# Performance work log

Hardware: AMD Instinct MI355X
Metric: run time of the kernel (lower is better)

Reference implementation:

```python
import jax, jax.numpy as jnp
import numpy as np

EPS = 1e-5
ROPE_BASE = 10000.0
N_HEAD = 16


def rms_norm(x, eps=EPS):
    return x * jax.lax.rsqrt(jnp.mean(x * x, axis=-1, keepdims=True) + eps)


def rope(x):
    # x: [B, H, L, D]; non-standard interleaved variant from the source:
    # x_odd = x[..., 1::2], x_even = x[..., ::2]
    # y = interleave(y_odd, y_even)
    B, H, L, D = x.shape
    inv_freq = 1.0 / (ROPE_BASE ** (jnp.arange(0, D, 2, dtype=jnp.float32) / D))
    angles = jnp.arange(L, dtype=jnp.float32)[:, None] * inv_freq[None, :]  # [L, D/2]
    cos, sin = jnp.cos(angles), jnp.sin(angles)
    x_odd = x[..., 1::2].astype(jnp.float32)
    x_even = x[..., ::2].astype(jnp.float32)
    y_odd = x_odd * cos - x_even * sin
    y_even = x_odd * sin + x_even * cos
    y = jnp.stack([y_odd, y_even], axis=-1).reshape(B, H, L, D)
    return y.astype(x.dtype)


def setup_inputs() -> dict:
    key = jax.random.key(0)
    k1, k2, k3 = jax.random.split(key, 3)
    B, L, HID = 2, 2048, 2048
    in_std = 0.5 * HID ** (-0.5)
    bound = (3 ** 0.5) * in_std
    x = jax.random.normal(k1, (B, L, HID), dtype=jnp.float32)
    W_qkv = jax.random.uniform(k2, (3 * HID, HID), minval=-bound, maxval=bound, dtype=jnp.float32)
    # out_proj is zero-initialized in the source; use small random weights so the
    # output (and gradients) are non-trivial for correctness checking.
    W_out = jax.random.uniform(k3, (HID, HID), minval=-bound, maxval=bound, dtype=jnp.float32)
    return {"x": x, "W_qkv": W_qkv, "W_out": W_out}


def reference(x, W_qkv, W_out):
    B, L, HID = x.shape
    D = HID // N_HEAD
    qkv = jnp.einsum('blc,fc->blf', x, W_qkv)  # [B, L, 3*HID]
    q, k, v = jnp.split(qkv, 3, axis=-1)
    def heads(t):
        return t.reshape(B, L, N_HEAD, D).transpose(0, 2, 1, 3)  # [B,H,L,D]
    q, k, v = heads(q), heads(k), heads(v)
    q = rope(rms_norm(q))
    k = rope(rms_norm(k))
    scale = 1.0 / jnp.sqrt(jnp.asarray(D, dtype=jnp.float32))
    scores = jnp.einsum('bhqd,bhkd->bhqk', q, k) * scale
    causal = jnp.tril(jnp.ones((L, L), dtype=bool))
    scores = jnp.where(causal, scores, -jnp.inf)
    attn = jax.nn.softmax(scores, axis=-1)
    out = jnp.einsum('bhqk,bhkd->bhqd', attn, v)
    out = out.transpose(0, 2, 1, 3).reshape(B, L, HID)
    return jnp.einsum('blc,fc->blf', out, W_out)
```

## Files before the change

kernel.cpp:

```cpp
#include <hip/hip_runtime.h>
#include <stdint.h>
#include <math.h>

typedef unsigned short u16;
typedef unsigned int u32;
typedef __attribute__((ext_vector_type(8))) short bf16x8;
typedef __attribute__((ext_vector_type(4))) float f32x4;

#define SEQ 2048
#define HID 2048
#define NH  16
#define DH  128
#define NB  2

typedef __attribute__((address_space(1))) const u32 gu32;
typedef __attribute__((address_space(3))) u32 lu32;

__device__ __forceinline__ u16 f2bf(float f) {
  u32 u = __float_as_uint(f);
  return (u16)((u + 0x7fffu + ((u >> 16) & 1u)) >> 16);
}
__device__ __forceinline__ float bf2f(u16 h) { return __uint_as_float(((u32)h) << 16); }

__device__ __forceinline__ void gload_lds16(const void* g, void* l) {
  __builtin_amdgcn_global_load_lds((gu32*)g, (lu32*)l, 16, 0, 0);
}

__global__ __launch_bounds__(256) void k_cvt3(const float* __restrict__ s0, u16* __restrict__ d0, int n0,
                                              const float* __restrict__ s1, u16* __restrict__ d1, int n1,
                                              const float* __restrict__ s2, u16* __restrict__ d2, int n2) {
  int i = blockIdx.x * 256 + threadIdx.x;
  int stride = gridDim.x * 256;
  int total = n0 + n1 + n2;
  for (; i < total; i += stride) {
    const float* s; u16* d; int k = i;
    if (k < n0) { s = s0; d = d0; }
    else if (k < n0 + n1) { s = s1; d = d1; k -= n0; }
    else { s = s2; d = d2; k -= n0 + n1; }
    float4 v = ((const float4*)s)[k];
    ushort4 o;
    o.x = f2bf(v.x); o.y = f2bf(v.y); o.z = f2bf(v.z); o.w = f2bf(v.w);
    ((ushort4*)d)[k] = o;
  }
}

template<int EPI>
__global__ __launch_bounds__(256)
void k_gemm(const u16* __restrict__ A, const u16* __restrict__ Bm,
            float* __restrict__ Cf, u16* __restrict__ Qr, u16* __restrict__ Kr, u16* __restrict__ Vr,
            int N, int K, int NX) {
  __shared__ alignas(16) char sA[128 * 128];
  __shared__ alignas(16) char sB[128 * 128];
  const int tid = threadIdx.x;
  const int wid = tid >> 6, lane = tid & 63;
  const int l15 = lane & 15, l4 = lane >> 4;
  const int nwg = gridDim.x, bid = blockIdx.x;
  const int wg = (bid & 7) * (nwg >> 3) + (bid >> 3);
  const int bx = wg % NX, by = wg / NX;
  const int m0 = by * 128, n0 = bx * 128;
  const int wr = (wid >> 1) * 64, wc = (wid & 1) * 64;

  f32x4 acc[4][4];
  #pragma unroll
  for (int i = 0; i < 4; ++i)
    #pragma unroll
    for (int j = 0; j < 4; ++j)
      acc[i][j] = (f32x4){0.f, 0.f, 0.f, 0.f};

  const int nkt = K >> 6;
  for (int kt = 0; kt < nkt; ++kt) {
    const int k0 = kt << 6;
    __syncthreads();
    #pragma unroll
    for (int it = 0; it < 4; ++it) {
      int o = it * 4096 + tid * 16;
      int row = o >> 7, cb = o & 127;
      int scb = cb ^ ((row & 7) << 4);
      gload_lds16((const char*)A + ((size_t)(m0 + row) * K + k0) * 2 + scb, &sA[it * 4096 + wid * 1024]);
    }
    #pragma unroll
    for (int it = 0; it < 4; ++it) {
      int o = it * 4096 + tid * 16;
      int row = o >> 7, cb = o & 127;
      int scb = cb ^ ((row & 7) << 4);
      gload_lds16((const char*)Bm + ((size_t)(n0 + row) * K + k0) * 2 + scb, &sB[it * 4096 + wid * 1024]);
    }
    __syncthreads();
    #pragma unroll
    for (int kk = 0; kk < 2; ++kk) {
      bf16x8 av[4], bv[4];
      #pragma unroll
      for (int mi = 0; mi < 4; ++mi) {
        int row = wr + mi * 16 + l15;
        int colb = kk * 64 + 16 * l4;
        av[mi] = *(const bf16x8*)&sA[row * 128 + (colb ^ ((row & 7) << 4))];
      }
      #pragma unroll
      for (int ni = 0; ni < 4; ++ni) {
        int row = wc + ni * 16 + l15;
        int colb = kk * 64 + 16 * l4;
        bv[ni] = *(const bf16x8*)&sB[row * 128 + (colb ^ ((row & 7) << 4))];
      }
      #pragma unroll
      for (int mi = 0; mi < 4; ++mi)
        #pragma unroll
        for (int ni = 0; ni < 4; ++ni)
          acc[mi][ni] = __builtin_amdgcn_mfma_f32_16x16x32_bf16(av[mi], bv[ni], acc[mi][ni], 0, 0, 0);
    }
  }

  #pragma unroll
  for (int mi = 0; mi < 4; ++mi) {
    #pragma unroll
    for (int ni = 0; ni < 4; ++ni) {
      #pragma unroll
      for (int j = 0; j < 4; ++j) {
        int gm = m0 + wr + mi * 16 + l4 * 4 + j;
        int gn = n0 + wc + ni * 16 + l15;
        float v = acc[mi][ni][j];
        if (EPI == 0) {
          int b = gm >> 11, l = gm & 2047;
          int which = gn >> 11, hid = gn & 2047;
          int h = hid >> 7, d = hid & 127;
          u16* dst = (which == 0) ? Qr : ((which == 1) ? Kr : Vr);
          size_t idx = ((size_t)(b * NH + h) * SEQ + l) * DH + d;
          dst[idx] = f2bf(v);
        } else {
          Cf[(size_t)gm * N + gn] = v;
        }
      }
    }
  }
}

__global__ __launch_bounds__(256) void k_vtr(const u16* __restrict__ Vr, u16* __restrict__ Vt) {
  __shared__ u16 tile[64][72];
  const int k0 = blockIdx.x * 64, d0 = blockIdx.y * 64, bh = blockIdx.z;
  const u16* src = Vr + ((size_t)bh << 18);
  u16* dst = Vt + ((size_t)bh << 18);
  const int tid = threadIdx.x;
  #pragma unroll
  for (int it = 0; it < 2; ++it) {
    int e = it * 2048 + tid * 8;
    int r = e >> 6, c = e & 63;
    bf16x8 v = *(const bf16x8*)(src + (size_t)(k0 + r) * DH + d0 + c);
    *(bf16x8*)&tile[r][c] = v;
  }
  __syncthreads();
  #pragma unroll
  for (int it = 0; it < 2; ++it) {
    int e = it * 2048 + tid * 8;
    int rd = e >> 6, ck = e & 63;
    bf16x8 w;
    #pragma unroll
    for (int i = 0; i < 8; ++i) w[i] = (short)tile[ck + i][rd];
    *(bf16x8*)(dst + (size_t)(d0 + rd) * SEQ + k0 + ck) = w;
  }
}

__global__ __launch_bounds__(256) void k_nrope2(u16* __restrict__ Qr, u16* __restrict__ Kr, float mq) {
  u16* T = blockIdx.y ? Kr : Qr;
  const float mul = blockIdx.y ? 1.0f : mq;
  const int r = blockIdx.x * 4 + (threadIdx.x >> 6);
  const int lane = threadIdx.x & 63;
  u16* p = T + ((size_t)r << 7) + lane * 2;
  u32 pr = *(const u32*)p;
  float xe = bf2f((u16)(pr & 0xffffu));
  float xo = bf2f((u16)(pr >> 16));
  float ss = xe * xe + xo * xo;
  #pragma unroll
  for (int off = 1; off < 64; off <<= 1) ss += __shfl_xor(ss, off);
  float rinv = rsqrtf(ss * (1.f / 128.f) + 1e-5f);
  float e = xe * rinv, o = xo * rinv;
  int pos = r & (SEQ - 1);
  float freq = exp2f(-0.20762050593046014f * (float)lane);
  float ang = (float)pos * freq;
  float sn, cs;
  sincosf(ang, &sn, &cs);
  u32 outw = (u32)f2bf((o * cs - e * sn) * mul) | ((u32)f2bf((o * sn + e * cs) * mul) << 16);
  *(u32*)p = outw;
}


__device__ __forceinline__ void smax(f32x4 (&sacc)[4], float& m_, float& se,
                                     f32x4* accO, u32 (&pw)[8],
                                     bool diag, int qpos, int kb, int l15, int l4) {
  if (diag) {
    #pragma unroll
    for (int sj = 0; sj < 4; ++sj)
      #pragma unroll
      for (int j = 0; j < 4; ++j) {
        int kpos = kb + sj * 16 + l4 * 4 + j;
        if (kpos > qpos) sacc[sj][j] = -1e30f;
      }
  }
  float mx = sacc[0][0];
  #pragma unroll
  for (int sj = 0; sj < 4; ++sj)
    #pragma unroll
    for (int j = 0; j < 4; ++j) mx = fmaxf(mx, sacc[sj][j]);
  mx = fmaxf(mx, __shfl_xor(mx, 16));
  mx = fmaxf(mx, __shfl_xor(mx, 32));
  if (!__all(mx <= m_ + 8.f)) {
    float mn = fmaxf(m_, mx);
    float corr = __builtin_exp2f(m_ - mn);
    m_ = mn;
    se *= corr;
    float corr4[4];
    #pragma unroll
    for (int j = 0; j < 4; ++j) corr4[j] = __shfl(corr, l4 * 4 + j);
    #pragma unroll
    for (int db = 0; db < 8; ++db) {
      f32x4 a = accO[db];
      #pragma unroll
      for (int j = 0; j < 4; ++j) a[j] *= corr4[j];
      accO[db] = a;
    }
  }
  float sum = 0.f;
  #pragma unroll
  for (int sj = 0; sj < 4; ++sj)
    #pragma unroll
    for (int jp = 0; jp < 2; ++jp) {
      float p0 = __builtin_exp2f(sacc[sj][jp * 2]     - m_);
      float p1 = __builtin_exp2f(sacc[sj][jp * 2 + 1] - m_);
      pw[sj * 2 + jp] = (u32)f2bf(p0) | ((u32)f2bf(p1) << 16);
      sum += p0 + p1;
    }
  sum += __shfl_xor(sum, 16);
  sum += __shfl_xor(sum, 32);
  se += sum;
}

__device__ __forceinline__ void pwrite(char* sPw, const u32 (&pw)[8], int l15, int l4) {
  const int sw = (l15 & 7) << 4;
  char* base = sPw + l15 * 128;
  #pragma unroll
  for (int sj = 0; sj < 4; ++sj)
    #pragma unroll
    for (int jp = 0; jp < 2; ++jp)
      *(u32*)(base + ((sj * 32 + l4 * 8 + jp * 4) ^ sw)) = pw[sj * 2 + jp];
}

__device__ __forceinline__ void stage_kv(const char* Kp, const char* Vtp, int kb,
                                         char* bK, char* bV, int tid, int wid) {
  #pragma unroll
  for (int it = 0; it < 4; ++it) {
    int o = it * 4096 + tid * 16;
    int row = o >> 8, cb = o & 255;
    int scb = cb ^ ((row & 7) << 4);
    gload_lds16(Kp + (size_t)(kb + row) * 256 + scb, &bK[it * 4096 + wid * 1024]);
  }
  #pragma unroll
  for (int it = 0; it < 4; ++it) {
    int o = it * 4096 + tid * 16;
    int row = o >> 7, cb = o & 127;
    int scb = cb ^ ((row & 7) << 4);
    gload_lds16(Vtp + (size_t)row * (SEQ * 2) + kb * 2 + scb, &bV[it * 4096 + wid * 1024]);
  }
}

__global__ __launch_bounds__(256, 2)
void k_attn(const u16* __restrict__ Q, const u16* __restrict__ Kg,
            const u16* __restrict__ Vt, u16* __restrict__ O) {
  __shared__ alignas(16) char sK0[64 * 256];
  __shared__ alignas(16) char sK1[64 * 256];
  __shared__ alignas(16) char sV0[128 * 128];
  __shared__ alignas(16) char sV1[128 * 128];
  __shared__ alignas(16) char sP[4 * 2048];
  const int tid = threadIdx.x, wid = tid >> 6, lane = tid & 63;
  const int l15 = lane & 15, l4 = lane >> 4;
  const int i = blockIdx.x;
  const int xcd = i & 7, slot = i >> 3;
  const int p = slot & 15;
  const int bh = xcd + 8 * (slot >> 4);
  const int b = bh >> 4, h = bh & 15;
  const int tA = p, tB = 31 - p;
  const u16* Qp = Q + ((size_t)bh << 18);
  const char* Kp = (const char*)(Kg + ((size_t)bh << 18));
  const char* Vtp = (const char*)(Vt + ((size_t)bh << 18));
  const int q0A = tA * 64 + wid * 16;
  const int q0B = tB * 64 + wid * 16;

  bf16x8 aqA[4], aqB[4];
  #pragma unroll
  for (int kk = 0; kk < 4; ++kk) {
    aqA[kk] = *(const bf16x8*)(Qp + (size_t)(q0A + l15) * DH + kk * 32 + 8 * l4);
    aqB[kk] = *(const bf16x8*)(Qp + (size_t)(q0B + l15) * DH + kk * 32 + 8 * l4);
  }

  f32x4 accA[8], accB[8];
  #pragma unroll
  for (int i2 = 0; i2 < 8; ++i2) { accA[i2] = (f32x4){0.f,0.f,0.f,0.f}; accB[i2] = (f32x4){0.f,0.f,0.f,0.f}; }
  float mA = -1e30f, mB = -1e30f, seA = 0.f, seB = 0.f;

  char* sPw = sP + wid * 2048;
  const int psw = (l15 & 7) << 4;
  const int nt = tB + 1;

  stage_kv(Kp, Vtp, 0, sK0, sV0, tid, wid);
  for (int t = 0; t < nt; ++t) {
    char* bK = (t & 1) ? sK1 : sK0;
    char* bV = (t & 1) ? sV1 : sV0;
    if (t + 1 < nt) {
      stage_kv(Kp, Vtp, (t + 1) << 6, (t & 1) ? sK0 : sK1, (t & 1) ? sV0 : sV1, tid, wid);
      asm volatile("s_waitcnt vmcnt(8)" ::: "memory");
    } else {
      asm volatile("s_waitcnt vmcnt(0)" ::: "memory");
    }
    __builtin_amdgcn_sched_barrier(0);
    __builtin_amdgcn_s_barrier();

    const int kb = t << 6;
    if (t <= tA) {
      f32x4 sb[4], sa[4];
      __builtin_amdgcn_s_setprio(1);
      #pragma unroll
      for (int sj = 0; sj < 4; ++sj) {
        sb[sj] = (f32x4){0.f,0.f,0.f,0.f};
        sa[sj] = (f32x4){0.f,0.f,0.f,0.f};
        int row = sj * 16 + l15;
        const char* rK = bK + (row << 8);
        int swr = (row & 7) << 4;
        #pragma unroll
        for (int kk = 0; kk < 4; ++kk) {
          bf16x8 bkv = *(const bf16x8*)(rK + ((kk * 64 + 16 * l4) ^ swr));
          sb[sj] = __builtin_amdgcn_mfma_f32_16x16x32_bf16(bkv, aqB[kk], sb[sj], 0, 0, 0);
          sa[sj] = __builtin_amdgcn_mfma_f32_16x16x32_bf16(bkv, aqA[kk], sa[sj], 0, 0, 0);
        }
      }
      __builtin_amdgcn_s_setprio(0);
      u32 pwB[8], pwA[8];
      smax(sb, mB, seB, accB, pwB, false, 0, kb, l15, l4);
      smax(sa, mA, seA, accA, pwA, t == tA, q0A + l15, kb, l15, l4);
      pwrite(sPw, pwB, l15, l4);
      bf16x8 paB0 = *(const bf16x8*)(sPw + l15 * 128 + ((16 * l4) ^ psw));
      bf16x8 paB1 = *(const bf16x8*)(sPw + l15 * 128 + ((64 + 16 * l4) ^ psw));
      pwrite(sPw, pwA, l15, l4);
      bf16x8 paA0 = *(const bf16x8*)(sPw + l15 * 128 + ((16 * l4) ^ psw));
      bf16x8 paA1 = *(const bf16x8*)(sPw + l15 * 128 + ((64 + 16 * l4) ^ psw));
      __builtin_amdgcn_s_setprio(1);
      #pragma unroll
      for (int db = 0; db < 8; ++db) {
        int row = db * 16 + l15;
        const char* vb = bV + row * 128;
        int swr = (row & 7) << 4;
        bf16x8 b0 = *(const bf16x8*)(vb + ((16 * l4) ^ swr));
        bf16x8 b1 = *(const bf16x8*)(vb + ((64 + 16 * l4) ^ swr));
        accB[db] = __builtin_amdgcn_mfma_f32_16x16x32_bf16(paB0, b0, accB[db], 0, 0, 0);
        accA[db] = __builtin_amdgcn_mfma_f32_16x16x32_bf16(paA0, b0, accA[db], 0, 0, 0);
        accB[db] = __builtin_amdgcn_mfma_f32_16x16x32_bf16(paB1, b1, accB[db], 0, 0, 0);
        accA[db] = __builtin_amdgcn_mfma_f32_16x16x32_bf16(paA1, b1, accA[db], 0, 0, 0);
      }
      __builtin_amdgcn_s_setprio(0);
    } else {
      f32x4 sb[4];
      __builtin_amdgcn_s_setprio(1);
      #pragma unroll
      for (int sj = 0; sj < 4; ++sj) {
        sb[sj] = (f32x4){0.f,0.f,0.f,0.f};
        int row = sj * 16 + l15;
        const char* rK = bK + (row << 8);
        int swr = (row & 7) << 4;
        #pragma unroll
        for (int kk = 0; kk < 4; ++kk) {
          bf16x8 bkv = *(const bf16x8*)(rK + ((kk * 64 + 16 * l4) ^ swr));
          sb[sj] = __builtin_amdgcn_mfma_f32_16x16x32_bf16(bkv, aqB[kk], sb[sj], 0, 0, 0);
        }
      }
      __builtin_amdgcn_s_setprio(0);
      u32 pwB[8];
      smax(sb, mB, seB, accB, pwB, t == tB, q0B + l15, kb, l15, l4);
      pwrite(sPw, pwB, l15, l4);
      bf16x8 paB0 = *(const bf16x8*)(sPw + l15 * 128 + ((16 * l4) ^ psw));
      bf16x8 paB1 = *(const bf16x8*)(sPw + l15 * 128 + ((64 + 16 * l4) ^ psw));
      __builtin_amdgcn_s_setprio(1);
      #pragma unroll
      for (int db = 0; db < 8; ++db) {
        int row = db * 16 + l15;
        const char* vb = bV + row * 128;
        int swr = (row & 7) << 4;
        bf16x8 b0 = *(const bf16x8*)(vb + ((16 * l4) ^ swr));
        bf16x8 b1 = *(const bf16x8*)(vb + ((64 + 16 * l4) ^ swr));
        accB[db] = __builtin_amdgcn_mfma_f32_16x16x32_bf16(paB0, b0, accB[db], 0, 0, 0);
        accB[db] = __builtin_amdgcn_mfma_f32_16x16x32_bf16(paB1, b1, accB[db], 0, 0, 0);
      }
      __builtin_amdgcn_s_setprio(0);
    }

    __builtin_amdgcn_s_barrier();
  }

  float seA4[4], seB4[4];
  #pragma unroll
  for (int j = 0; j < 4; ++j) {
    seA4[j] = __shfl(seA, l4 * 4 + j);
    seB4[j] = __shfl(seB, l4 * 4 + j);
  }
  #pragma unroll
  for (int db = 0; db < 8; ++db) {
    #pragma unroll
    for (int j = 0; j < 4; ++j) {
      int d = db * 16 + l15;
      int qA = q0A + l4 * 4 + j;
      int qB = q0B + l4 * 4 + j;
      O[(size_t)(b * SEQ + qA) * HID + h * DH + d] = f2bf(accA[db][j] / seA4[j]);
      O[(size_t)(b * SEQ + qB) * HID + h * DH + d] = f2bf(accB[db][j] / seB4[j]);
    }
  }
}

extern "C" void kernel_launch(void* const* d_in, const int* in_sizes, int n_in,
                              void* d_out, int out_size, void* d_ws, size_t ws_size,
                              hipStream_t stream) {
  (void)in_sizes; (void)n_in; (void)out_size; (void)ws_size;
  const float* x = (const float*)d_in[0];
  const float* Wqkv = (const float*)d_in[1];
  const float* Wout = (const float*)d_in[2];
  float* out = (float*)d_out;
  char* ws = (char*)d_ws;

  u16* xb  = (u16*)(ws);
  u16* wqb = (u16*)(ws + (size_t)16777216);
  u16* Vt  = wqb;
  u16* wob = (u16*)(ws + (size_t)16777216 + 25165824);
  u16* Qr  = (u16*)(ws + (size_t)50331648);
  u16* Kr  = Qr + (size_t)8388608;
  u16* Vr  = Kr + (size_t)8388608;
  u16* Ob  = xb;

  const float mq = 0.08838834764831845f * 1.4426950408889634f;

  k_cvt3<<<dim3(2048), dim3(256), 0, stream>>>(x, xb, (NB * SEQ * HID) / 4,
                                               Wqkv, wqb, (3 * HID * HID) / 4,
                                               Wout, wob, (HID * HID) / 4);

  k_gemm<0><<<dim3(1536), dim3(256), 0, stream>>>(xb, wqb, nullptr, Qr, Kr, Vr, 3 * HID, HID, 48);

  k_vtr<<<dim3(SEQ / 64, DH / 64, NB * NH), dim3(256), 0, stream>>>(Vr, Vt);
  k_nrope2<<<dim3((NB * NH * SEQ) / 4, 2), dim3(256), 0, stream>>>(Qr, Kr, mq);

  k_attn<<<dim3(512), dim3(256), 0, stream>>>(Qr, Kr, Vt, Ob);

  k_gemm<1><<<dim3(512), dim3(256), 0, stream>>>(Ob, wob, out, nullptr, nullptr, nullptr, HID, HID, 16);
}
```

Before: 298.8 us.

## Rewrite GEMM as 128x256-tile, 8-wave double-buffered pipelined kernel

Replaces the single-buffered 128x128 GEMM, which synchronised around every K step, with a 512-thread kernel computing 128x256 tiles. Shared-memory A/B buffers are double-buffered so global-to-LDS loads for the next K chunk overlap MFMA work, using explicit vmcnt/lgkmcnt waits, s_barrier, sched_barrier and s_setprio around the MFMA phases. Both the QKV and output projections use it, with grids halved to match the larger tiles. The hand-tuned wait counts and barriers add correctness risk, and the larger tiles mean fewer workgroups, which could under-fill the GPU for the smaller output GEMM.

Measured after the change: 311.3 us. +4.2%, slower.

```diff
diff --git a/kernel.cpp b/kernel.cpp
--- a/kernel.cpp
+++ b/kernel.cpp
@@ -45,68 +45,133 @@
 }
 
 template<int EPI>
-__global__ __launch_bounds__(256)
-void k_gemm(const u16* __restrict__ A, const u16* __restrict__ Bm,
-            float* __restrict__ Cf, u16* __restrict__ Qr, u16* __restrict__ Kr, u16* __restrict__ Vr,
-            int N, int K, int NX) {
-  __shared__ alignas(16) char sA[128 * 128];
-  __shared__ alignas(16) char sB[128 * 128];
+__global__ __launch_bounds__(512, 2)
+void k_gemm4(const u16* __restrict__ A, const u16* __restrict__ Bm,
+             float* __restrict__ Cf, u16* __restrict__ Qr, u16* __restrict__ Kr, u16* __restrict__ Vr,
+             int N, int K, int NX) {
+  __shared__ alignas(16) char sA0[16384];
+  __shared__ alignas(16) char sA1[16384];
+  __shared__ alignas(16) char sB0[32768];
+  __shared__ alignas(16) char sB1[32768];
   const int tid = threadIdx.x;
   const int wid = tid >> 6, lane = tid & 63;
   const int l15 = lane & 15, l4 = lane >> 4;
+  const int wm = wid >> 2, wn = wid & 3;
   const int nwg = gridDim.x, bid = blockIdx.x;
   const int wg = (bid & 7) * (nwg >> 3) + (bid >> 3);
   const int bx = wg % NX, by = wg / NX;
-  const int m0 = by * 128, n0 = bx * 128;
-  const int wr = (wid >> 1) * 64, wc = (wid & 1) * 64;
+  const int m0 = by * 128, n0 = bx * 256;
+  const char* Ab = (const char*)A;
+  const char* Bb = (const char*)Bm;
+  const size_t rs = (size_t)K * 2;
+
+  int aoff[4][2], boff[4][2];
+  #pragma unroll
+  for (int mm = 0; mm < 4; ++mm)
+    #pragma unroll
+    for (int ks = 0; ks < 2; ++ks) {
+      int row = wm * 64 + mm * 16 + l15;
+      aoff[mm][ks] = row * 128 + ((ks * 64 + 16 * l4) ^ ((row & 7) << 4));
+    }
+  #pragma unroll
+  for (int nn = 0; nn < 4; ++nn)
+    #pragma unroll
+    for (int ks = 0; ks < 2; ++ks) {
+      int row = wn * 64 + nn * 16 + l15;
+      boff[nn][ks] = row * 128 + ((ks * 64 + 16 * l4) ^ ((row & 7) << 4));
+    }
 
   f32x4 acc[4][4];
   #pragma unroll
   for (int i = 0; i < 4; ++i)
     #pragma unroll
-    for (int j = 0; j < 4; ++j)
-      acc[i][j] = (f32x4){0.f, 0.f, 0.f, 0.f};
-
-  const int nkt = K >> 6;
-  for (int kt = 0; kt < nkt; ++kt) {
-    const int k0 = kt << 6;
-    __syncthreads();
-    #pragma unroll
-    for (int it = 0; it < 4; ++it) {
-      int o = it * 4096 + tid * 16;
+    for (int jx = 0; jx < 4; ++jx) acc[i][jx] = (f32x4){0.f, 0.f, 0.f, 0.f};
+  bf16x8 areg[4][2], breg[4][2];
+
+  auto STG1 = [&](const char* src, char* dst) {
+    int o = tid * 16;
+    int row = o >> 7, cb = o & 127;
+    gload_lds16(src + (size_t)row * rs + (cb ^ ((row & 7) << 4)), dst + wid * 1024);
+  };
+  auto STG2 = [&](const char* src, char* dst) {
+    #pragma unroll
+    for (int jj = 0; jj < 2; ++jj) {
+      int o = jj * 8192 + tid * 16;
       int row = o >> 7, cb = o & 127;
-      int scb = cb ^ ((row & 7) << 4);
-      gload_lds16((const char*)A + ((size_t)(m0 + row) * K + k0) * 2 + scb, &sA[it * 4096 + wid * 1024]);
-    }
-    #pragma unroll
-    for (int it = 0; it < 4; ++it) {
-      int o = it * 4096 + tid * 16;
-      int row = o >> 7, cb = o & 127;
-      int scb = cb ^ ((row & 7) << 4);
-      gload_lds16((const char*)Bm + ((size_t)(n0 + row) * K + k0) * 2 + scb, &sB[it * 4096 + wid * 1024]);
-    }
-    __syncthreads();
-    #pragma unroll
-    for (int kk = 0; kk < 2; ++kk) {
-      bf16x8 av[4], bv[4];
-      #pragma unroll
-      for (int mi = 0; mi < 4; ++mi) {
-        int row = wr + mi * 16 + l15;
-        int colb = kk * 64 + 16 * l4;
-        av[mi] = *(const bf16x8*)&sA[row * 128 + (colb ^ ((row & 7) << 4))];
-      }
-      #pragma unroll
-      for (int ni = 0; ni < 4; ++ni) {
-        int row = wc + ni * 16 + l15;
-        int colb = kk * 64 + 16 * l4;
-        bv[ni] = *(const bf16x8*)&sB[row * 128 + (colb ^ ((row & 7) << 4))];
-      }
-      #pragma unroll
-      for (int mi = 0; mi < 4; ++mi)
-        #pragma unroll
-        for (int ni = 0; ni < 4; ++ni)
-          acc[mi][ni] = __builtin_amdgcn_mfma_f32_16x16x32_bf16(av[mi], bv[ni], acc[mi][ni], 0, 0, 0);
-    }
+      gload_lds16(src + (size_t)row * rs + (cb ^ ((row & 7) << 4)), dst + jj * 8192 + wid * 1024);
+    }
+  };
+  auto RD = [&](const char* sA, const char* sB) {
+    #pragma unroll
+    for (int mm = 0; mm < 4; ++mm)
+      #pragma unroll
+      for (int ks = 0; ks < 2; ++ks) areg[mm][ks] = *(const bf16x8*)(sA + aoff[mm][ks]);
+    #pragma unroll
+    for (int nn = 0; nn < 4; ++nn)
+      #pragma unroll
+      for (int ks = 0; ks < 2; ++ks) breg[nn][ks] = *(const bf16x8*)(sB + boff[nn][ks]);
+  };
+  auto MF = [&](int ks) {
+    #pragma unroll
+    for (int mm = 0; mm < 4; ++mm)
+      #pragma unroll
+      for (int nn = 0; nn < 4; ++nn)
+        acc[mm][nn] = __builtin_amdgcn_mfma_f32_16x16x32_bf16(areg[mm][ks], breg[nn][ks], acc[mm][nn], 0, 0, 0);
+  };
+
+  const int NIT = K >> 7;
+  STG2(Bb + (size_t)n0 * rs, sB0);
+  STG2(Bb + (size_t)(n0 + 128) * rs, sB0 + 16384);
+  STG1(Ab + (size_t)m0 * rs, sA0);
+  STG1(Ab + (size_t)(m0 + 64) * rs, sA0 + 8192);
+  STG2(Bb + (size_t)n0 * rs + 128, sB1);
+  STG2(Bb + (size_t)(n0 + 128) * rs + 128, sB1 + 16384);
+  STG1(Ab + (size_t)m0 * rs + 128, sA1);
+  asm volatile("s_waitcnt vmcnt(5)" ::: "memory");
+  __builtin_amdgcn_sched_barrier(0);
+  __builtin_amdgcn_s_barrier();
+
+  for (int j = 0; j < NIT; ++j) {
+    const size_t k1 = (size_t)(2 * j + 1) * 128;
+    const size_t k2 = (size_t)(2 * j + 2) * 128;
+    const size_t k3 = (size_t)(2 * j + 3) * 128;
+    const bool g2 = (j + 1 < NIT);
+    RD(sA0, sB0);
+    STG1(Ab + (size_t)(m0 + 64) * rs + k1, sA1 + 8192);
+    __builtin_amdgcn_s_barrier();
+    asm volatile("s_waitcnt lgkmcnt(0)" ::: "memory");
+    __builtin_amdgcn_sched_barrier(0);
+    __builtin_amdgcn_s_setprio(1); MF(0); __builtin_amdgcn_s_setprio(0);
+    __builtin_amdgcn_s_barrier();
+    if (g2) {
+      STG2(Bb + (size_t)n0 * rs + k2, sB0);
+      STG2(Bb + (size_t)(n0 + 128) * rs + k2, sB0 + 16384);
+      STG1(Ab + (size_t)m0 * rs + k2, sA0);
+    }
+    __builtin_amdgcn_s_barrier();
+    __builtin_amdgcn_s_setprio(1); MF(1); __builtin_amdgcn_s_setprio(0);
+    if (g2) { asm volatile("s_waitcnt vmcnt(5)" ::: "memory"); }
+    else    { asm volatile("s_waitcnt vmcnt(0)" ::: "memory"); }
+    __builtin_amdgcn_sched_barrier(0);
+    __builtin_amdgcn_s_barrier();
+    RD(sA1, sB1);
+    if (g2) STG1(Ab + (size_t)(m0 + 64) * rs + k2, sA0 + 8192);
+    __builtin_amdgcn_s_barrier();
+    asm volatile("s_waitcnt lgkmcnt(0)" ::: "memory");
+    __builtin_amdgcn_sched_barrier(0);
+    __builtin_amdgcn_s_setprio(1); MF(0); __builtin_amdgcn_s_setprio(0);
+    __builtin_amdgcn_s_barrier();
+    if (g2) {
+      STG2(Bb + (size_t)n0 * rs + k3, sB1);
+      STG2(Bb + (size_t)(n0 + 128) * rs + k3, sB1 + 16384);
+      STG1(Ab + (size_t)m0 * rs + k3, sA1);
+    }
+    __builtin_amdgcn_s_barrier();
+    __builtin_amdgcn_s_setprio(1); MF(1); __builtin_amdgcn_s_setprio(0);
+    if (g2) { asm volatile("s_waitcnt vmcnt(5)" ::: "memory"); }
+    else    { asm volatile("s_waitcnt vmcnt(0)" ::: "memory"); }
+    __builtin_amdgcn_sched_barrier(0);
+    __builtin_amdgcn_s_barrier();
   }
 
   #pragma unroll
@@ -114,17 +179,16 @@
     #pragma unroll
     for (int ni = 0; ni < 4; ++ni) {
       #pragma unroll
-      for (int j = 0; j < 4; ++j) {
-        int gm = m0 + wr + mi * 16 + l4 * 4 + j;
-        int gn = n0 + wc + ni * 16 + l15;
-        float v = acc[mi][ni][j];
+      for (int jj = 0; jj < 4; ++jj) {
+        int gm = m0 + wm * 64 + mi * 16 + l4 * 4 + jj;
+        int gn = n0 + wn * 64 + ni * 16 + l15;
+        float v = acc[mi][ni][jj];
         if (EPI == 0) {
           int b = gm >> 11, l = gm & 2047;
           int which = gn >> 11, hid = gn & 2047;
           int h = hid >> 7, d = hid & 127;
           u16* dst = (which == 0) ? Qr : ((which == 1) ? Kr : Vr);
-          size_t idx = ((size_t)(b * NH + h) * SEQ + l) * DH + d;
-          dst[idx] = f2bf(v);
+          dst[((size_t)(b * NH + h) * SEQ + l) * DH + d] = f2bf(v);
         } else {
           Cf[(size_t)gm * N + gn] = v;
         }
@@ -180,7 +244,6 @@
   u32 outw = (u32)f2bf((o * cs - e * sn) * mul) | ((u32)f2bf((o * sn + e * cs) * mul) << 16);
   *(u32*)p = outw;
 }
-
 
 __device__ __forceinline__ void smax(f32x4 (&sacc)[4], float& m_, float& se,
                                      f32x4* accO, u32 (&pw)[8],
@@ -435,12 +498,12 @@
                                                Wqkv, wqb, (3 * HID * HID) / 4,
                                                Wout, wob, (HID * HID) / 4);
 
-  k_gemm<0><<<dim3(1536), dim3(256), 0, stream>>>(xb, wqb, nullptr, Qr, Kr, Vr, 3 * HID, HID, 48);
+  k_gemm4<0><<<dim3(768), dim3(512), 0, stream>>>(xb, wqb, nullptr, Qr, Kr, Vr, 3 * HID, HID, 24);
 
   k_vtr<<<dim3(SEQ / 64, DH / 64, NB * NH), dim3(256), 0, stream>>>(Vr, Vt);
   k_nrope2<<<dim3((NB * NH * SEQ) / 4, 2), dim3(256), 0, stream>>>(Qr, Kr, mq);
 
   k_attn<<<dim3(512), dim3(256), 0, stream>>>(Qr, Kr, Vt, Ob);
 
-  k_gemm<1><<<dim3(512), dim3(256), 0, stream>>>(Ob, wob, out, nullptr, nullptr, nullptr, HID, HID, 16);
-}
+  k_gemm4<1><<<dim3(256), dim3(512), 0, stream>>>(Ob, wob, out, nullptr, nullptr, nullptr, HID, HID, 8);
+}
```

## Load V tiles directly from global into registers instead of LDS staging

Applied to the files above, without the earlier changes.

Removes the double-buffered LDS staging of V in the attention kernel. Each wave now loads its V operand fragments straight from global memory into registers after the QK^T MFMAs, and the async wait count is reduced to match K-only staging. This frees 32KB of LDS and removes the LDS reads for V. In exchange, every wave redundantly fetches the same V tile from global/L2, global load latency sits on the PV path, and register pressure rises.

Measured after the change: 414.4 us. 38.7% more time.

```diff
diff --git a/kernel.cpp b/kernel.cpp
--- a/kernel.cpp
+++ b/kernel.cpp
@@ -181,7 +181,6 @@
   *(u32*)p = outw;
 }
 
-
 __device__ __forceinline__ void smax(f32x4 (&sacc)[4], float& m_, float& se,
                                      f32x4* accO, u32 (&pw)[8],
                                      bool diag, int qpos, int kb, int l15, int l4) {
@@ -242,8 +241,7 @@
       *(u32*)(base + ((sj * 32 + l4 * 8 + jp * 4) ^ sw)) = pw[sj * 2 + jp];
 }
 
-__device__ __forceinline__ void stage_kv(const char* Kp, const char* Vtp, int kb,
-                                         char* bK, char* bV, int tid, int wid) {
+__device__ __forceinline__ void stage_k(const char* Kp, int kb, char* bK, int tid, int wid) {
   #pragma unroll
   for (int it = 0; it < 4; ++it) {
     int o = it * 4096 + tid * 16;
@@ -251,13 +249,6 @@
     int scb = cb ^ ((row & 7) << 4);
     gload_lds16(Kp + (size_t)(kb + row) * 256 + scb, &bK[it * 4096 + wid * 1024]);
   }
-  #pragma unroll
-  for (int it = 0; it < 4; ++it) {
-    int o = it * 4096 + tid * 16;
-    int row = o >> 7, cb = o & 127;
-    int scb = cb ^ ((row & 7) << 4);
-    gload_lds16(Vtp + (size_t)row * (SEQ * 2) + kb * 2 + scb, &bV[it * 4096 + wid * 1024]);
-  }
 }
 
 __global__ __launch_bounds__(256, 2)
@@ -265,8 +256,6 @@
             const u16* __restrict__ Vt, u16* __restrict__ O) {
   __shared__ alignas(16) char sK0[64 * 256];
   __shared__ alignas(16) char sK1[64 * 256];
-  __shared__ alignas(16) char sV0[128 * 128];
-  __shared__ alignas(16) char sV1[128 * 128];
   __shared__ alignas(16) char sP[4 * 2048];
   const int tid = threadIdx.x, wid = tid >> 6, lane = tid & 63;
   const int l15 = lane & 15, l4 = lane >> 4;
@@ -278,7 +267,7 @@
   const int tA = p, tB = 31 - p;
   const u16* Qp = Q + ((size_t)bh << 18);
   const char* Kp = (const char*)(Kg + ((size_t)bh << 18));
-  const char* Vtp = (const char*)(Vt + ((size_t)bh << 18));
+  const u16* Vtp = Vt + ((size_t)bh << 18);
   const int q0A = tA * 64 + wid * 16;
   const int q0B = tB * 64 + wid * 16;
 
@@ -298,13 +287,12 @@
   const int psw = (l15 & 7) << 4;
   const int nt = tB + 1;
 
-  stage_kv(Kp, Vtp, 0, sK0, sV0, tid, wid);
+  stage_k(Kp, 0, sK0, tid, wid);
   for (int t = 0; t < nt; ++t) {
     char* bK = (t & 1) ? sK1 : sK0;
-    char* bV = (t & 1) ? sV1 : sV0;
     if (t + 1 < nt) {
-      stage_kv(Kp, Vtp, (t + 1) << 6, (t & 1) ? sK0 : sK1, (t & 1) ? sV0 : sV1, tid, wid);
-      asm volatile("s_waitcnt vmcnt(8)" ::: "memory");
+      stage_k(Kp, (t + 1) << 6, (t & 1) ? sK0 : sK1, tid, wid);
+      asm volatile("s_waitcnt vmcnt(4)" ::: "memory");
     } else {
       asm volatile("s_waitcnt vmcnt(0)" ::: "memory");
     }
@@ -330,6 +318,13 @@
         }
       }
       __builtin_amdgcn_s_setprio(0);
+      bf16x8 vr0[8], vr1[8];
+      #pragma unroll
+      for (int db = 0; db < 8; ++db) {
+        const u16* vp = Vtp + (size_t)(db * 16 + l15) * SEQ + kb + 8 * l4;
+        vr0[db] = *(const bf16x8*)vp;
+        vr1[db] = *(const bf16x8*)(vp + 32);
+      }
       u32 pwB[8], pwA[8];
       smax(sb, mB, seB, accB, pwB, false, 0, kb, l15, l4);
       smax(sa, mA, seA, accA, pwA, t == tA, q0A + l15, kb, l15, l4);
@@ -342,15 +337,10 @@
       __builtin_amdgcn_s_setprio(1);
       #pragma unroll
       for (int db = 0; db < 8; ++db) {
-        int row = db * 16 + l15;
-        const char* vb = bV + row * 128;
-        int swr = (row & 7) << 4;
-        bf16x8 b0 = *(const bf16x8*)(vb + ((16 * l4) ^ swr));
-        bf16x8 b1 = *(const bf16x8*)(vb + ((64 + 16 * l4) ^ swr));
-        accB[db] = __builtin_amdgcn_mfma_f32_16x16x32_bf16(paB0, b0, accB[db], 0, 0, 0);
-        accA[db] = __builtin_amdgcn_mfma_f32_16x16x32_bf16(paA0, b0, accA[db], 0, 0, 0);
-        accB[db] = __builtin_amdgcn_mfma_f32_16x16x32_bf16(paB1, b1, accB[db], 0, 0, 0);
-        accA[db] = __builtin_amdgcn_mfma_f32_16x16x32_bf16(paA1, b1, accA[db], 0, 0, 0);
+        accB[db] = __builtin_amdgcn_mfma_f32_16x16x32_bf16(paB0, vr0[db], accB[db], 0, 0, 0);
+        accA[db] = __builtin_amdgcn_mfma_f32_16x16x32_bf16(paA0, vr0[db], accA[db], 0, 0, 0);
+        accB[db] = __builtin_amdgcn_mfma_f32_16x16x32_bf16(paB1, vr1[db], accB[db], 0, 0, 0);
+        accA[db] = __builtin_amdgcn_mfma_f32_16x16x32_bf16(paA1, vr1[db], accA[db], 0, 0, 0);
       }
       __builtin_amdgcn_s_setprio(0);
     } else {
@@ -369,6 +359,13 @@
         }
       }
       __builtin_amdgcn_s_setprio(0);
+      bf16x8 vr0[8], vr1[8];
+      #pragma unroll
+      for (int db = 0; db < 8; ++db) {
+        const u16* vp = Vtp + (size_t)(db * 16 + l15) * SEQ + kb + 8 * l4;
+        vr0[db] = *(const bf16x8*)vp;
+        vr1[db] = *(const bf16x8*)(vp + 32);
+      }
       u32 pwB[8];
       smax(sb, mB, seB, accB, pwB, t == tB, q0B + l15, kb, l15, l4);
       pwrite(sPw, pwB, l15, l4);
@@ -377,13 +374,8 @@
       __builtin_amdgcn_s_setprio(1);
       #pragma unroll
       for (int db = 0; db < 8; ++db) {
-        int row = db * 16 + l15;
-        const char* vb = bV + row * 128;
-        int swr = (row & 7) << 4;
-        bf16x8 b0 = *(const bf16x8*)(vb + ((16 * l4) ^ swr));
-        bf16x8 b1 = *(const bf16x8*)(vb + ((64 + 16 * l4) ^ swr));
-        accB[db] = __builtin_amdgcn_mfma_f32_16x16x32_bf16(paB0, b0, accB[db], 0, 0, 0);
-        accB[db] = __builtin_amdgcn_mfma_f32_16x16x32_bf16(paB1, b1, accB[db], 0, 0, 0);
+        accB[db] = __builtin_amdgcn_mfma_f32_16x16x32_bf16(paB0, vr0[db], accB[db], 0, 0, 0);
+        accB[db] = __builtin_amdgcn_mfma_f32_16x16x32_bf16(paB1, vr1[db], accB[db], 0, 0, 0);
       }
       __builtin_amdgcn_s_setprio(0);
     }
```
